# Optimization experiments

Measured on AMD Instinct MI355X. Metric: run time of the kernel, lower is better.

The kernel has to match this reference:

```python
import jax, jax.numpy as jnp
import numpy as np

B, N, C, L = 32, 1024, 1024, 16  # batch, pixels (HW), channels, visual tokens


def setup_inputs() -> dict:
    key = jax.random.key(0)
    ks = jax.random.split(key, 18)
    s = lambda fan_in: 1.0 / np.sqrt(fan_in)
    def lin(kw, kb, fin, fout):
        W = jax.random.uniform(kw, (fin, fout), jnp.float32, -s(fin), s(fin))
        b = jax.random.uniform(kb, (fout,), jnp.float32, -s(fin), s(fin))
        return W, b
    tok_W, tok_b = lin(ks[0], ks[1], C, L)          # tokenizer pointwise conv
    key_W, key_b = lin(ks[2], ks[3], C, C // 2)     # transformer key proj
    query_W, query_b = lin(ks[4], ks[5], C, C // 2) # transformer query proj
    f1_W, f1_b = lin(ks[6], ks[7], C, C)            # FFN 1
    f2_W, f2_b = lin(ks[8], ks[9], C, C)            # FFN 2
    q_W, q_b = lin(ks[10], ks[11], C, C)            # projector W_q
    k_W, k_b = lin(ks[12], ks[13], C, C)            # projector W_k
    feature_map = jax.random.normal(ks[14], (B, N, C), jnp.float32)
    T_in = jnp.zeros((B, L, C), jnp.float32)  # unused by FilterBasedTokenizer
    return dict(feature_map=feature_map, T_in=T_in,
                tok_W=tok_W, tok_b=tok_b, key_W=key_W, key_b=key_b,
                query_W=query_W, query_b=query_b, f1_W=f1_W, f1_b=f1_b,
                f2_W=f2_W, f2_b=f2_b, q_W=q_W, q_b=q_b, k_W=k_W, k_b=k_b)


def reference(feature_map, T_in, tok_W, tok_b, key_W, key_b, query_W, query_b,
              f1_W, f1_b, f2_W, f2_b, q_W, q_b, k_W, k_b):
    X = feature_map  # [B, N, C]
    # --- FilterBasedTokenizer: softmax over pixel dim, aggregate pixels -> tokens
    proj = X @ tok_W + tok_b                         # [B, N, L]
    attn = jax.nn.softmax(proj, axis=1)              # softmax over N (dim=1)
    T = jnp.einsum('bnl,bnc->blc', attn, X)          # [B, L, C]
    # --- Transformer block on visual tokens
    k = T @ key_W + key_b                            # [B, L, C/2]
    q = T @ query_W + query_b                        # [B, L, C/2]
    scores = jnp.einsum('bld,bmd->blm', k, q)        # [B, L, L]
    T_dash = T + jax.nn.softmax(scores, axis=2) @ T  # self-attn residual
    T_out = T_dash + (jax.nn.relu(T_dash @ f1_W + f1_b) @ f2_W + f2_b)
    # --- Projector: pixels attend to tokens
    sim = jnp.einsum('bnc,blc->bnl', X @ q_W + q_b, T_out @ k_W + k_b)  # [B, N, L]
    X_out = X + jax.nn.softmax(sim, axis=2) @ T_out  # [B, N, C]
    return (X_out, T_out)
```

## Files before the change

### kernel.cpp

```cpp
#include <hip/hip_runtime.h>
#include <hip/hip_bf16.h>
#include <stdint.h>

#define BB 32
#define NN 1024
#define CC 1024
#define LL 16

typedef __attribute__((ext_vector_type(4))) float f32x4;
typedef __attribute__((ext_vector_type(8))) short short8;
typedef __attribute__((ext_vector_type(4))) unsigned short ushort4v;

__device__ __forceinline__ unsigned short f2bf(float f) {
  union { float f; unsigned u; } v; v.f = f;
  unsigned r = v.u + 0x7FFF + ((v.u >> 16) & 1);
  return (unsigned short)(r >> 16);
}
__device__ __forceinline__ float bf2f(unsigned short h) {
  union { unsigned u; float f; } v; v.u = ((unsigned)h) << 16; return v.f;
}

__global__ __launch_bounds__(256) void wprep(
    const float* __restrict__ keyW, const float* __restrict__ queryW,
    const float* __restrict__ f1W, const float* __restrict__ f2W,
    const float* __restrict__ kW, const float* __restrict__ qW,
    const float* __restrict__ tokW, const float* __restrict__ keyb,
    const float* __restrict__ queryb,
    unsigned short* __restrict__ WkqT, unsigned short* __restrict__ f1WT,
    unsigned short* __restrict__ f2WT, unsigned short* __restrict__ kWT,
    unsigned short* __restrict__ qWbf, unsigned short* __restrict__ tokWT,
    float* __restrict__ biaskq)
{
  int z = blockIdx.z;
  int tx = threadIdx.x, ty = threadIdx.y;
  if (z == 5) {
    int gid = (blockIdx.y * 32 + blockIdx.x) * 256 + ty * 32 + tx;
    if (gid < 16384) {
      int l = gid >> 10, c = gid & 1023;
      tokWT[gid] = f2bf(tokW[c * 16 + l]);
    } else if (gid < 17408) {
      int i = gid - 16384;
      biaskq[i] = (i < 512) ? keyb[i] : queryb[i - 512];
    }
    return;
  }
  if (z == 4) {
#pragma unroll
    for (int i = 0; i < 4; ++i) {
      int row = blockIdx.y * 32 + ty + 8 * i;
      int col = blockIdx.x * 32 + tx;
      qWbf[row * 1024 + col] = f2bf(qW[row * 1024 + col]);
    }
    return;
  }
  __shared__ float tile[32][33];
  int j0 = blockIdx.x * 32, k0 = blockIdx.y * 32;
  const float* src = (z == 1) ? f1W : (z == 2) ? f2W : kW;
#pragma unroll
  for (int i = 0; i < 4; ++i) {
    int k = k0 + ty + 8 * i;
    int j = j0 + tx;
    float v;
    if (z == 0) v = (j < 512) ? keyW[k * 512 + j] : queryW[k * 512 + (j - 512)];
    else        v = src[k * 1024 + j];
    tile[ty + 8 * i][tx] = v;
  }
  __syncthreads();
  unsigned short* dst = (z == 0) ? WkqT : (z == 1) ? f1WT : (z == 2) ? f2WT : kWT;
#pragma unroll
  for (int i = 0; i < 4; ++i) {
    int j = j0 + ty + 8 * i;
    dst[j * 1024 + k0 + tx] = f2bf(tile[tx][ty + 8 * i]);
  }
}

__global__ __launch_bounds__(256) void proj_mfma(
    const float* __restrict__ X, const unsigned short* __restrict__ Wt,
    const float* __restrict__ bias, float* __restrict__ out)
{
  __shared__ __align__(16) char sp[16384];
  int tid = threadIdx.x, wid = tid >> 6, lane = tid & 63;
  int lr = lane & 15, hi = lane >> 4;
  int pix0 = blockIdx.x * 64;
  int b = pix0 >> 10;
  int row = tid >> 2, seg = tid & 3;
  const float* xr = X + (size_t)(pix0 + row) * 1024 + seg * 32;
  const unsigned short* Wb = Wt + (size_t)lr * 1024 + hi * 8;
  int wbyte[4];
#pragma unroll
  for (int u = 0; u < 4; ++u)
    wbyte[u] = row * 256 + (((seg * 64 + u * 16) ^ ((row & 7) << 4)));
  int arow = wid * 16 + lr;
  int rbyte = arow * 256;
  int rx = (arow & 7) << 4;
  f32x4 acc = (f32x4)0.f;
  for (int k0 = 0; k0 < 1024; k0 += 128) {
    f32x4 v[8];
#pragma unroll
    for (int i = 0; i < 8; ++i) v[i] = *(const f32x4*)(xr + k0 + i * 4);
    __syncthreads();
#pragma unroll
    for (int u = 0; u < 4; ++u) {
      short8 pk;
      pk[0] = (short)f2bf(v[2*u][0]);   pk[1] = (short)f2bf(v[2*u][1]);
      pk[2] = (short)f2bf(v[2*u][2]);   pk[3] = (short)f2bf(v[2*u][3]);
      pk[4] = (short)f2bf(v[2*u+1][0]); pk[5] = (short)f2bf(v[2*u+1][1]);
      pk[6] = (short)f2bf(v[2*u+1][2]); pk[7] = (short)f2bf(v[2*u+1][3]);
      *(short8*)(sp + wbyte[u]) = pk;
    }
    __syncthreads();
#pragma unroll
    for (int kk = 0; kk < 4; ++kk) {
      short8 af = *(const short8*)(sp + rbyte + (((kk * 64 + hi * 16) ^ rx)));
      short8 bf = *(const short8*)(Wb + k0 + kk * 32);
      acc = __builtin_amdgcn_mfma_f32_16x16x32_bf16(af, bf, acc, 0, 0, 0);
    }
  }
  int pixb = pix0 + wid * 16 + hi * 4;
  float bv = bias[lr];
#pragma unroll
  for (int rr = 0; rr < 4; ++rr) {
    int pix = pixb + rr;
    out[((size_t)b * 16 + lr) * 1024 + (pix & 1023)] = acc[rr] + bv;
  }
}

__global__ __launch_bounds__(256) void softmax_n(float* __restrict__ projT) {
  float* row = projT + (size_t)blockIdx.x * NN;
  int t = threadIdx.x;
  f32x4 v = ((f32x4*)row)[t];
  float m = fmaxf(fmaxf(v[0], v[1]), fmaxf(v[2], v[3]));
#pragma unroll
  for (int msk = 32; msk >= 1; msk >>= 1) m = fmaxf(m, __shfl_xor(m, msk));
  __shared__ float redm[4], reds[4];
  if ((t & 63) == 0) redm[t >> 6] = m;
  __syncthreads();
  m = fmaxf(fmaxf(redm[0], redm[1]), fmaxf(redm[2], redm[3]));
  f32x4 e;
  e[0] = __expf(v[0] - m); e[1] = __expf(v[1] - m);
  e[2] = __expf(v[2] - m); e[3] = __expf(v[3] - m);
  float s = e[0] + e[1] + e[2] + e[3];
#pragma unroll
  for (int msk = 32; msk >= 1; msk >>= 1) s += __shfl_xor(s, msk);
  if ((t & 63) == 0) reds[t >> 6] = s;
  __syncthreads();
  s = reds[0] + reds[1] + reds[2] + reds[3];
  float inv = 1.f / s;
  e[0] *= inv; e[1] *= inv; e[2] *= inv; e[3] *= inv;
  ((f32x4*)row)[t] = e;
}

__global__ __launch_bounds__(256) void tpart_kernel(
    const float* __restrict__ X, const float* __restrict__ attnT,
    unsigned short* __restrict__ TpartBf)
{
  int b = blockIdx.y, ch = blockIdx.x;
  int n0 = ch * 128;
  __shared__ float att[128][16];
  int tid = threadIdx.x;
#pragma unroll
  for (int i = 0; i < 2; ++i) {
    int fi = tid + 256 * i;
    int l = fi >> 5, n4 = (fi & 31) << 2;
    f32x4 a = *(const f32x4*)&attnT[((size_t)b * 16 + l) * 1024 + n0 + n4];
    att[n4 + 0][l] = a[0]; att[n4 + 1][l] = a[1];
    att[n4 + 2][l] = a[2]; att[n4 + 3][l] = a[3];
  }
  __syncthreads();
  f32x4 acc[16];
#pragma unroll
  for (int l = 0; l < 16; ++l) acc[l] = (f32x4)0.f;
  const float* xp = X + ((size_t)b * 1024 + n0) * 1024 + tid * 4;
#pragma unroll 4
  for (int n = 0; n < 128; ++n) {
    f32x4 xv = *(const f32x4*)(xp + (size_t)n * 1024);
    const f32x4* ar = (const f32x4*)&att[n][0];
    f32x4 a0 = ar[0], a1 = ar[1], a2 = ar[2], a3 = ar[3];
    acc[0]  += a0[0]*xv; acc[1]  += a0[1]*xv; acc[2]  += a0[2]*xv; acc[3]  += a0[3]*xv;
    acc[4]  += a1[0]*xv; acc[5]  += a1[1]*xv; acc[6]  += a1[2]*xv; acc[7]  += a1[3]*xv;
    acc[8]  += a2[0]*xv; acc[9]  += a2[1]*xv; acc[10] += a2[2]*xv; acc[11] += a2[3]*xv;
    acc[12] += a3[0]*xv; acc[13] += a3[1]*xv; acc[14] += a3[2]*xv; acc[15] += a3[3]*xv;
  }
  unsigned short* op = TpartBf + (size_t)(b * 8 + ch) * 16 * 1024 + tid * 4;
#pragma unroll
  for (int l = 0; l < 16; ++l) {
    f32x4 s = acc[l];
    ushort4v h; h[0]=f2bf(s[0]); h[1]=f2bf(s[1]); h[2]=f2bf(s[2]); h[3]=f2bf(s[3]);
    *(ushort4v*)(op + (size_t)l * 1024) = h;
  }
}

__global__ void treduce(const unsigned short* __restrict__ TpartBf,
                        float* __restrict__ T, unsigned short* __restrict__ Tbf) {
  int f = blockIdx.x * 256 + threadIdx.x;
  int b = f >> 12, w = f & 4095;
  f32x4 s = (f32x4)0.f;
#pragma unroll
  for (int ch = 0; ch < 8; ++ch) {
    ushort4v h = ((const ushort4v*)TpartBf)[(size_t)(b * 8 + ch) * 4096 + w];
    s[0] += bf2f(h[0]); s[1] += bf2f(h[1]); s[2] += bf2f(h[2]); s[3] += bf2f(h[3]);
  }
  ((f32x4*)T)[f] = s;
  ushort4v h; h[0]=f2bf(s[0]); h[1]=f2bf(s[1]); h[2]=f2bf(s[2]); h[3]=f2bf(s[3]);
  ((ushort4v*)Tbf)[f] = h;
}

template<int RELU, int HAS_BIAS, int HAS_RES, int STORE_F32, int STORE_BF16>
__global__ __launch_bounds__(256) void gemm32x64(
    const unsigned short* __restrict__ A, const unsigned short* __restrict__ Bm,
    const float* __restrict__ bias, const float* __restrict__ res,
    float* __restrict__ outF, unsigned short* __restrict__ outB)
{
  const int K = 1024;
  __shared__ __align__(16) char sh[12288];
  char* Asp = sh;
  char* Bsp = sh + 4096;
  int tid = threadIdx.x, wid = tid >> 6, lane = tid & 63;
  int lr = lane & 15, hi = lane >> 4;
  int m0 = blockIdx.x * 32, n0 = blockIdx.y * 64;
  int arow = tid >> 3, acol = (tid & 7) * 8;
  int brow = tid >> 2, bcol = (tid & 3) * 16;
  const unsigned short* Ap = A + (size_t)(m0 + arow) * K + acol;
  const unsigned short* Bp = Bm + (size_t)(n0 + brow) * K + bcol;
  int aw  = arow * 128 + (((acol * 2) ^ ((arow & 7) << 4)));
  int bw0 = brow * 128 + (((bcol * 2) ^ ((brow & 7) << 4)));
  int bw1 = brow * 128 + ((((bcol * 2) + 16) ^ ((brow & 7) << 4)));
  short8 aR[2]; short8 bR[2][2];
  aR[0]    = *(const short8*)(Ap);
  bR[0][0] = *(const short8*)(Bp);
  bR[0][1] = *(const short8*)(Bp + 8);
  aR[1]    = *(const short8*)(Ap + 64);
  bR[1][0] = *(const short8*)(Bp + 64);
  bR[1][1] = *(const short8*)(Bp + 72);
  f32x4 acc[2];
  acc[0] = (f32x4)0.f; acc[1] = (f32x4)0.f;
  int wm = (wid >> 1) * 16, wn = (wid & 1) * 32;
  int arb = (wm + lr) * 128, arx = ((wm + lr) & 7) << 4;
  for (int s = 0; s < 16; ++s) {
    __syncthreads();
    *(short8*)(Asp + aw)  = aR[s & 1];
    *(short8*)(Bsp + bw0) = bR[s & 1][0];
    *(short8*)(Bsp + bw1) = bR[s & 1][1];
    __syncthreads();
    if (s + 2 < 16) {
      int k0 = (s + 2) * 64;
      aR[s & 1]    = *(const short8*)(Ap + k0);
      bR[s & 1][0] = *(const short8*)(Bp + k0);
      bR[s & 1][1] = *(const short8*)(Bp + k0 + 8);
    }
#pragma unroll
    for (int kk = 0; kk < 2; ++kk) {
      short8 af = *(const short8*)(Asp + arb + (((kk * 64 + hi * 16) ^ arx)));
#pragma unroll
      for (int sn = 0; sn < 2; ++sn) {
        int br = wn + sn * 16 + lr;
        short8 bf = *(const short8*)(Bsp + br * 128 + (((kk * 64 + hi * 16) ^ ((br & 7) << 4))));
        acc[sn] = __builtin_amdgcn_mfma_f32_16x16x32_bf16(af, bf, acc[sn], 0, 0, 0);
      }
    }
  }
  int row0 = m0 + wm + hi * 4;
#pragma unroll
  for (int sn = 0; sn < 2; ++sn) {
    int col = n0 + wn + sn * 16 + lr;
    float bv_ = HAS_BIAS ? bias[col] : 0.f;
#pragma unroll
    for (int rr = 0; rr < 4; ++rr) {
      float x = acc[sn][rr] + bv_;
      if (RELU) x = fmaxf(x, 0.f);
      size_t idx = (size_t)(row0 + rr) * 1024 + col;
      if (HAS_RES) x += res[idx];
      if (STORE_F32) outF[idx] = x;
      if (STORE_BF16) outB[idx] = f2bf(x);
    }
  }
}

__global__ __launch_bounds__(256) void scores_tdash(
    const float* __restrict__ kq, const float* __restrict__ T,
    float* __restrict__ Tdash, unsigned short* __restrict__ Tdbf)
{
  int cs = blockIdx.x, b = blockIdx.y;
  int c0 = cs * 128;
  __shared__ float Ts[16][128];
  int tid = threadIdx.x, lane = tid & 63;
#pragma unroll
  for (int i = 0; i < 2; ++i) {
    int fi = tid + 256 * i;
    int rrow = fi >> 5, c4 = (fi & 31) * 4;
    *(f32x4*)&Ts[rrow][c4] = *(const f32x4*)&T[((size_t)b * 16 + rrow) * 1024 + c0 + c4];
  }
  __syncthreads();
  int l = tid >> 4, m = tid & 15;
  const float* krow = kq + ((size_t)b * 16 + l) * 1024;
  const float* qrow = kq + ((size_t)b * 16 + m) * 1024 + 512;
  float s = 0.f;
#pragma unroll 8
  for (int d = 0; d < 512; d += 4) {
    f32x4 kv = *(const f32x4*)(krow + d);
    f32x4 qv = *(const f32x4*)(qrow + d);
    s += kv[0]*qv[0] + kv[1]*qv[1] + kv[2]*qv[2] + kv[3]*qv[3];
  }
  float mx = s;
  mx = fmaxf(mx, __shfl_xor(mx, 1)); mx = fmaxf(mx, __shfl_xor(mx, 2));
  mx = fmaxf(mx, __shfl_xor(mx, 4)); mx = fmaxf(mx, __shfl_xor(mx, 8));
  float e = __expf(s - mx);
  float sum = e;
  sum += __shfl_xor(sum, 1); sum += __shfl_xor(sum, 2);
  sum += __shfl_xor(sum, 4); sum += __shfl_xor(sum, 8);
  float pv = e / sum;
  float pl[16];
#pragma unroll
  for (int i = 0; i < 16; ++i) pl[i] = __shfl(pv, (lane & 48) + i);
  float* od = Tdash + ((size_t)b * 16 + l) * 1024 + c0;
  unsigned short* ob = Tdbf + ((size_t)b * 16 + l) * 1024 + c0;
#pragma unroll
  for (int h = 0; h < 2; ++h) {
    int c = m * 8 + h * 4;
    f32x4 o = *(const f32x4*)&Ts[l][c];
#pragma unroll
    for (int mm = 0; mm < 16; ++mm) {
      f32x4 tv = *(const f32x4*)&Ts[mm][c];
      o += pl[mm] * tv;
    }
    *(f32x4*)(od + c) = o;
    ushort4v hh; hh[0]=f2bf(o[0]); hh[1]=f2bf(o[1]); hh[2]=f2bf(o[2]); hh[3]=f2bf(o[3]);
    *(ushort4v*)(ob + c) = hh;
  }
}

__global__ __launch_bounds__(256) void r_kernel(
    const unsigned short* __restrict__ Tkbf, const float* __restrict__ qb,
    float* __restrict__ r)
{
  int row = blockIdx.x * 4 + (threadIdx.x >> 6);
  int lane = threadIdx.x & 63;
  const unsigned short* p = Tkbf + (size_t)row * CC;
  float s = 0.f;
#pragma unroll
  for (int h = 0; h < 2; ++h) {
    int d0 = lane * 8 + h * 512;
    short8 v = *(const short8*)&p[d0];
#pragma unroll
    for (int jj = 0; jj < 8; ++jj)
      s += bf2f((unsigned short)v[jj]) * qb[d0 + jj];
  }
#pragma unroll
  for (int msk = 32; msk >= 1; msk >>= 1) s += __shfl_xor(s, msk);
  if (lane == 0) r[row] = s;
}

__global__ __launch_bounds__(256) void sim_out_kernel(
    const float* __restrict__ X, const unsigned short* __restrict__ Gt,
    const float* __restrict__ rbias, const float* __restrict__ Tout,
    float* __restrict__ Xout)
{
  __shared__ __align__(16) char sp[16384];
  __shared__ float Ps[64][16];
  int tid = threadIdx.x, wid = tid >> 6, lane = tid & 63;
  int lr = lane & 15, hi = lane >> 4;
  int pix0 = blockIdx.x * 64 + blockIdx.y * 1024;
  int b = blockIdx.y;
  int row = tid >> 2, seg = tid & 3;
  const float* xr = X + (size_t)(pix0 + row) * 1024 + seg * 32;
  const unsigned short* Wb = Gt + (size_t)b * 16 * 1024 + (size_t)lr * 1024 + hi * 8;
  int wbyte[4];
#pragma unroll
  for (int u = 0; u < 4; ++u)
    wbyte[u] = row * 256 + (((seg * 64 + u * 16) ^ ((row & 7) << 4)));
  int arow = wid * 16 + lr;
  int rbyte = arow * 256;
  int rx = (arow & 7) << 4;
  f32x4 acc = (f32x4)0.f;
  for (int k0 = 0; k0 < 1024; k0 += 128) {
    f32x4 v[8];
#pragma unroll
    for (int i = 0; i < 8; ++i) v[i] = *(const f32x4*)(xr + k0 + i * 4);
    __syncthreads();
#pragma unroll
    for (int u = 0; u < 4; ++u) {
      short8 pk;
      pk[0] = (short)f2bf(v[2*u][0]);   pk[1] = (short)f2bf(v[2*u][1]);
      pk[2] = (short)f2bf(v[2*u][2]);   pk[3] = (short)f2bf(v[2*u][3]);
      pk[4] = (short)f2bf(v[2*u+1][0]); pk[5] = (short)f2bf(v[2*u+1][1]);
      pk[6] = (short)f2bf(v[2*u+1][2]); pk[7] = (short)f2bf(v[2*u+1][3]);
      *(short8*)(sp + wbyte[u]) = pk;
    }
    __syncthreads();
#pragma unroll
    for (int kk = 0; kk < 4; ++kk) {
      short8 af = *(const short8*)(sp + rbyte + (((kk * 64 + hi * 16) ^ rx)));
      short8 bf = *(const short8*)(Wb + k0 + kk * 32);
      acc = __builtin_amdgcn_mfma_f32_16x16x32_bf16(af, bf, acc, 0, 0, 0);
    }
  }
  float bv = rbias[b * 16 + lr];
  int prow = wid * 16 + hi * 4;
#pragma unroll
  for (int rr = 0; rr < 4; ++rr) {
    float vv = acc[rr] + bv;
    float mx = vv;
    mx = fmaxf(mx, __shfl_xor(mx, 1)); mx = fmaxf(mx, __shfl_xor(mx, 2));
    mx = fmaxf(mx, __shfl_xor(mx, 4)); mx = fmaxf(mx, __shfl_xor(mx, 8));
    float e = __expf(vv - mx);
    float ss = e;
    ss += __shfl_xor(ss, 1); ss += __shfl_xor(ss, 2);
    ss += __shfl_xor(ss, 4); ss += __shfl_xor(ss, 8);
    Ps[prow + rr][lr] = e / ss;
  }
  __syncthreads();
  int c4 = tid * 4;
  f32x4 tsr[16];
#pragma unroll
  for (int l = 0; l < 16; ++l)
    tsr[l] = *(const f32x4*)&Tout[((size_t)b * 16 + l) * 1024 + c4];
  const float* xp = X + (size_t)pix0 * 1024 + c4;
  float* op = Xout + (size_t)pix0 * 1024 + c4;
#pragma unroll 2
  for (int n = 0; n < 64; ++n) {
    f32x4 xv = *(const f32x4*)(xp + (size_t)n * 1024);
    const f32x4* pr = (const f32x4*)&Ps[n][0];
    f32x4 p0 = pr[0], p1 = pr[1], p2 = pr[2], p3 = pr[3];
    f32x4 o = xv;
    o += p0[0]*tsr[0];  o += p0[1]*tsr[1];  o += p0[2]*tsr[2];  o += p0[3]*tsr[3];
    o += p1[0]*tsr[4];  o += p1[1]*tsr[5];  o += p1[2]*tsr[6];  o += p1[3]*tsr[7];
    o += p2[0]*tsr[8];  o += p2[1]*tsr[9];  o += p2[2]*tsr[10]; o += p2[3]*tsr[11];
    o += p3[0]*tsr[12]; o += p3[1]*tsr[13]; o += p3[2]*tsr[14]; o += p3[3]*tsr[15];
    *(f32x4*)(op + (size_t)n * 1024) = o;
  }
}

extern "C" void kernel_launch(void* const* d_in, const int* in_sizes, int n_in,
                              void* d_out, int out_size, void* d_ws, size_t ws_size,
                              hipStream_t stream)
{
  const float* X      = (const float*)d_in[0];
  const float* tokW   = (const float*)d_in[2];
  const float* tokB   = (const float*)d_in[3];
  const float* keyW   = (const float*)d_in[4];
  const float* keyB   = (const float*)d_in[5];
  const float* queryW = (const float*)d_in[6];
  const float* queryB = (const float*)d_in[7];
  const float* f1W    = (const float*)d_in[8];
  const float* f1B    = (const float*)d_in[9];
  const float* f2W    = (const float*)d_in[10];
  const float* f2B    = (const float*)d_in[11];
  const float* qW     = (const float*)d_in[12];
  const float* qB     = (const float*)d_in[13];
  const float* kW     = (const float*)d_in[14];
  const float* kB     = (const float*)d_in[15];

  float* Xout = (float*)d_out;
  float* Tout = (float*)d_out + (size_t)BB * NN * CC;

  char* ws = (char*)d_ws;
  size_t off = 0;
  auto alloc_f = [&](size_t n) { float* pp = (float*)(ws + off); off += n * 4; return pp; };
  float* attn   = alloc_f(524288);
  float* Tbuf   = alloc_f(524288);
  float* kqbuf  = alloc_f(524288);
  float* Tdash  = alloc_f(524288);
  float* rbuf   = alloc_f(1024);
  float* biaskq = alloc_f(1024);
  auto alloc_h = [&](size_t n) { unsigned short* pp = (unsigned short*)(ws + off); off += n * 2; return pp; };
  unsigned short* TpartBf = alloc_h(4194304);
  unsigned short* Tbf    = alloc_h(524288);
  unsigned short* Tdbf   = alloc_h(524288);
  unsigned short* Hbf    = alloc_h(524288);
  unsigned short* Toutbf = alloc_h(524288);
  unsigned short* Tkbf   = alloc_h(524288);
  unsigned short* Gtbf   = alloc_h(524288);
  unsigned short* WkqT   = alloc_h(1048576);
  unsigned short* f1WT   = alloc_h(1048576);
  unsigned short* f2WT   = alloc_h(1048576);
  unsigned short* kWT    = alloc_h(1048576);
  unsigned short* qWbf   = alloc_h(1048576);
  unsigned short* tokWT  = alloc_h(16384);
  (void)ws_size; (void)in_sizes; (void)n_in; (void)out_size;

  wprep<<<dim3(32, 32, 6), dim3(32, 8), 0, stream>>>(keyW, queryW, f1W, f2W, kW, qW,
                                                     tokW, keyB, queryB,
                                                     WkqT, f1WT, f2WT, kWT, qWbf, tokWT, biaskq);
  proj_mfma<<<dim3(512), 256, 0, stream>>>(X, tokWT, tokB, attn);
  softmax_n<<<512, 256, 0, stream>>>(attn);
  tpart_kernel<<<dim3(8, 32), 256, 0, stream>>>(X, attn, TpartBf);
  treduce<<<512, 256, 0, stream>>>(TpartBf, Tbuf, Tbf);
  gemm32x64<0,1,0,1,0><<<dim3(16, 16), 256, 0, stream>>>(Tbf, WkqT, biaskq, nullptr, kqbuf, nullptr);
  scores_tdash<<<dim3(8, 32), 256, 0, stream>>>(kqbuf, Tbuf, Tdash, Tdbf);
  gemm32x64<1,1,0,0,1><<<dim3(16, 16), 256, 0, stream>>>(Tdbf, f1WT, f1B, nullptr, nullptr, Hbf);
  gemm32x64<0,1,1,1,1><<<dim3(16, 16), 256, 0, stream>>>(Hbf, f2WT, f2B, Tdash, Tout, Toutbf);
  gemm32x64<0,1,0,0,1><<<dim3(16, 16), 256, 0, stream>>>(Toutbf, kWT, kB, nullptr, nullptr, Tkbf);
  r_kernel<<<128, 256, 0, stream>>>(Tkbf, qB, rbuf);
  gemm32x64<0,0,0,0,1><<<dim3(16, 16), 256, 0, stream>>>(Tkbf, qWbf, nullptr, nullptr, nullptr, Gtbf);
  sim_out_kernel<<<dim3(16, 32), 256, 0, stream>>>(X, Gtbf, rbuf, Tout, Xout);
}
```

Measured before the change: 210.6 us.

## Replace LDS-staged MFMA tiles with direct-register loads across kernels; split token reduction finer

The projection and sim kernels now feed MFMA straight from global memory, converting fp32 X to bf16 in registers instead of staging through swizzled LDS with barriers. The small GEMMs use a 16x16-per-wave direct-load tile instead of the 32x64 LDS double-buffered tile, doubling the grid. The token aggregation is split into 16 chunks of 64 pixels with batched loads, which doubles the partial buffer and the reduction work. Xout is written with nontemporal stores to avoid polluting cache. The aim is to remove LDS traffic and synchronisation and raise parallelism, at the cost of uncoalesced 32-byte-strided global reads and less operand reuse.

Result: slower. 230.3 us (+9.4%).

```diff
diff --git a/kernel.cpp b/kernel.cpp
--- a/kernel.cpp
+++ b/kernel.cpp
@@ -18,6 +18,14 @@
 }
 __device__ __forceinline__ float bf2f(unsigned short h) {
   union { unsigned u; float f; } v; v.u = ((unsigned)h) << 16; return v.f;
+}
+__device__ __forceinline__ short8 cvt8(f32x4 a, f32x4 b) {
+  short8 r;
+  r[0] = (short)f2bf(a[0]); r[1] = (short)f2bf(a[1]);
+  r[2] = (short)f2bf(a[2]); r[3] = (short)f2bf(a[3]);
+  r[4] = (short)f2bf(b[0]); r[5] = (short)f2bf(b[1]);
+  r[6] = (short)f2bf(b[2]); r[7] = (short)f2bf(b[3]);
+  return r;
 }
 
 __global__ __launch_bounds__(256) void wprep(
@@ -74,55 +82,29 @@
   }
 }
 
-__global__ __launch_bounds__(256) void proj_mfma(
-    const float* __restrict__ X, const unsigned short* __restrict__ Wt,
-    const float* __restrict__ bias, float* __restrict__ out)
-{
-  __shared__ __align__(16) char sp[16384];
+__global__ __launch_bounds__(256) void proj_direct(
+    const float* __restrict__ X, const unsigned short* __restrict__ tokWT,
+    const float* __restrict__ tokB, float* __restrict__ attn)
+{
   int tid = threadIdx.x, wid = tid >> 6, lane = tid & 63;
   int lr = lane & 15, hi = lane >> 4;
-  int pix0 = blockIdx.x * 64;
+  int pix0 = (blockIdx.x * 4 + wid) * 16;
   int b = pix0 >> 10;
-  int row = tid >> 2, seg = tid & 3;
-  const float* xr = X + (size_t)(pix0 + row) * 1024 + seg * 32;
-  const unsigned short* Wb = Wt + (size_t)lr * 1024 + hi * 8;
-  int wbyte[4];
-#pragma unroll
-  for (int u = 0; u < 4; ++u)
-    wbyte[u] = row * 256 + (((seg * 64 + u * 16) ^ ((row & 7) << 4)));
-  int arow = wid * 16 + lr;
-  int rbyte = arow * 256;
-  int rx = (arow & 7) << 4;
+  const float* Ar = X + (size_t)(pix0 + lr) * 1024 + hi * 8;
+  const unsigned short* Br = tokWT + lr * 1024 + hi * 8;
   f32x4 acc = (f32x4)0.f;
-  for (int k0 = 0; k0 < 1024; k0 += 128) {
-    f32x4 v[8];
-#pragma unroll
-    for (int i = 0; i < 8; ++i) v[i] = *(const f32x4*)(xr + k0 + i * 4);
-    __syncthreads();
-#pragma unroll
-    for (int u = 0; u < 4; ++u) {
-      short8 pk;
-      pk[0] = (short)f2bf(v[2*u][0]);   pk[1] = (short)f2bf(v[2*u][1]);
-      pk[2] = (short)f2bf(v[2*u][2]);   pk[3] = (short)f2bf(v[2*u][3]);
-      pk[4] = (short)f2bf(v[2*u+1][0]); pk[5] = (short)f2bf(v[2*u+1][1]);
-      pk[6] = (short)f2bf(v[2*u+1][2]); pk[7] = (short)f2bf(v[2*u+1][3]);
-      *(short8*)(sp + wbyte[u]) = pk;
-    }
-    __syncthreads();
-#pragma unroll
-    for (int kk = 0; kk < 4; ++kk) {
-      short8 af = *(const short8*)(sp + rbyte + (((kk * 64 + hi * 16) ^ rx)));
-      short8 bf = *(const short8*)(Wb + k0 + kk * 32);
-      acc = __builtin_amdgcn_mfma_f32_16x16x32_bf16(af, bf, acc, 0, 0, 0);
-    }
-  }
-  int pixb = pix0 + wid * 16 + hi * 4;
-  float bv = bias[lr];
-#pragma unroll
-  for (int rr = 0; rr < 4; ++rr) {
-    int pix = pixb + rr;
-    out[((size_t)b * 16 + lr) * 1024 + (pix & 1023)] = acc[rr] + bv;
-  }
+#pragma unroll 4
+  for (int k0 = 0; k0 < 1024; k0 += 32) {
+    f32x4 x0 = *(const f32x4*)(Ar + k0);
+    f32x4 x1 = *(const f32x4*)(Ar + k0 + 4);
+    short8 bfrag = *(const short8*)(Br + k0);
+    acc = __builtin_amdgcn_mfma_f32_16x16x32_bf16(cvt8(x0, x1), bfrag, acc, 0, 0, 0);
+  }
+  float bv = tokB[lr];
+  int pixb = pix0 + hi * 4;
+#pragma unroll
+  for (int rr = 0; rr < 4; ++rr)
+    attn[((size_t)b * 16 + lr) * 1024 + ((pixb + rr) & 1023)] = acc[rr] + bv;
 }
 
 __global__ __launch_bounds__(256) void softmax_n(float* __restrict__ projT) {
@@ -155,13 +137,11 @@
     unsigned short* __restrict__ TpartBf)
 {
   int b = blockIdx.y, ch = blockIdx.x;
-  int n0 = ch * 128;
-  __shared__ float att[128][16];
+  int n0 = ch * 64;
+  __shared__ float att[64][16];
   int tid = threadIdx.x;
-#pragma unroll
-  for (int i = 0; i < 2; ++i) {
-    int fi = tid + 256 * i;
-    int l = fi >> 5, n4 = (fi & 31) << 2;
+  {
+    int l = tid >> 4, n4 = (tid & 15) * 4;
     f32x4 a = *(const f32x4*)&attnT[((size_t)b * 16 + l) * 1024 + n0 + n4];
     att[n4 + 0][l] = a[0]; att[n4 + 1][l] = a[1];
     att[n4 + 2][l] = a[2]; att[n4 + 3][l] = a[3];
@@ -171,17 +151,22 @@
 #pragma unroll
   for (int l = 0; l < 16; ++l) acc[l] = (f32x4)0.f;
   const float* xp = X + ((size_t)b * 1024 + n0) * 1024 + tid * 4;
-#pragma unroll 4
-  for (int n = 0; n < 128; ++n) {
-    f32x4 xv = *(const f32x4*)(xp + (size_t)n * 1024);
-    const f32x4* ar = (const f32x4*)&att[n][0];
-    f32x4 a0 = ar[0], a1 = ar[1], a2 = ar[2], a3 = ar[3];
-    acc[0]  += a0[0]*xv; acc[1]  += a0[1]*xv; acc[2]  += a0[2]*xv; acc[3]  += a0[3]*xv;
-    acc[4]  += a1[0]*xv; acc[5]  += a1[1]*xv; acc[6]  += a1[2]*xv; acc[7]  += a1[3]*xv;
-    acc[8]  += a2[0]*xv; acc[9]  += a2[1]*xv; acc[10] += a2[2]*xv; acc[11] += a2[3]*xv;
-    acc[12] += a3[0]*xv; acc[13] += a3[1]*xv; acc[14] += a3[2]*xv; acc[15] += a3[3]*xv;
-  }
-  unsigned short* op = TpartBf + (size_t)(b * 8 + ch) * 16 * 1024 + tid * 4;
+  for (int nb = 0; nb < 64; nb += 8) {
+    f32x4 xv[8];
+#pragma unroll
+    for (int i = 0; i < 8; ++i) xv[i] = *(const f32x4*)(xp + (size_t)(nb + i) * 1024);
+#pragma unroll
+    for (int i = 0; i < 8; ++i) {
+      const f32x4* ar = (const f32x4*)&att[nb + i][0];
+      f32x4 a0 = ar[0], a1 = ar[1], a2 = ar[2], a3 = ar[3];
+      f32x4 x0 = xv[i];
+      acc[0]  += a0[0]*x0; acc[1]  += a0[1]*x0; acc[2]  += a0[2]*x0; acc[3]  += a0[3]*x0;
+      acc[4]  += a1[0]*x0; acc[5]  += a1[1]*x0; acc[6]  += a1[2]*x0; acc[7]  += a1[3]*x0;
+      acc[8]  += a2[0]*x0; acc[9]  += a2[1]*x0; acc[10] += a2[2]*x0; acc[11] += a2[3]*x0;
+      acc[12] += a3[0]*x0; acc[13] += a3[1]*x0; acc[14] += a3[2]*x0; acc[15] += a3[3]*x0;
+    }
+  }
+  unsigned short* op = TpartBf + (size_t)(b * 16 + ch) * 16 * 1024 + tid * 4;
 #pragma unroll
   for (int l = 0; l < 16; ++l) {
     f32x4 s = acc[l];
@@ -196,8 +181,8 @@
   int b = f >> 12, w = f & 4095;
   f32x4 s = (f32x4)0.f;
 #pragma unroll
-  for (int ch = 0; ch < 8; ++ch) {
-    ushort4v h = ((const ushort4v*)TpartBf)[(size_t)(b * 8 + ch) * 4096 + w];
+  for (int ch = 0; ch < 16; ++ch) {
+    ushort4v h = ((const ushort4v*)TpartBf)[(size_t)(b * 16 + ch) * 4096 + w];
     s[0] += bf2f(h[0]); s[1] += bf2f(h[1]); s[2] += bf2f(h[2]); s[3] += bf2f(h[3]);
   }
   ((f32x4*)T)[f] = s;
@@ -206,73 +191,35 @@
 }
 
 template<int RELU, int HAS_BIAS, int HAS_RES, int STORE_F32, int STORE_BF16>
-__global__ __launch_bounds__(256) void gemm32x64(
+__global__ __launch_bounds__(256) void gemm_direct(
     const unsigned short* __restrict__ A, const unsigned short* __restrict__ Bm,
     const float* __restrict__ bias, const float* __restrict__ res,
     float* __restrict__ outF, unsigned short* __restrict__ outB)
 {
-  const int K = 1024;
-  __shared__ __align__(16) char sh[12288];
-  char* Asp = sh;
-  char* Bsp = sh + 4096;
   int tid = threadIdx.x, wid = tid >> 6, lane = tid & 63;
   int lr = lane & 15, hi = lane >> 4;
-  int m0 = blockIdx.x * 32, n0 = blockIdx.y * 64;
-  int arow = tid >> 3, acol = (tid & 7) * 8;
-  int brow = tid >> 2, bcol = (tid & 3) * 16;
-  const unsigned short* Ap = A + (size_t)(m0 + arow) * K + acol;
-  const unsigned short* Bp = Bm + (size_t)(n0 + brow) * K + bcol;
-  int aw  = arow * 128 + (((acol * 2) ^ ((arow & 7) << 4)));
-  int bw0 = brow * 128 + (((bcol * 2) ^ ((brow & 7) << 4)));
-  int bw1 = brow * 128 + ((((bcol * 2) + 16) ^ ((brow & 7) << 4)));
-  short8 aR[2]; short8 bR[2][2];
-  aR[0]    = *(const short8*)(Ap);
-  bR[0][0] = *(const short8*)(Bp);
-  bR[0][1] = *(const short8*)(Bp + 8);
-  aR[1]    = *(const short8*)(Ap + 64);
-  bR[1][0] = *(const short8*)(Bp + 64);
-  bR[1][1] = *(const short8*)(Bp + 72);
-  f32x4 acc[2];
-  acc[0] = (f32x4)0.f; acc[1] = (f32x4)0.f;
-  int wm = (wid >> 1) * 16, wn = (wid & 1) * 32;
-  int arb = (wm + lr) * 128, arx = ((wm + lr) & 7) << 4;
-  for (int s = 0; s < 16; ++s) {
-    __syncthreads();
-    *(short8*)(Asp + aw)  = aR[s & 1];
-    *(short8*)(Bsp + bw0) = bR[s & 1][0];
-    *(short8*)(Bsp + bw1) = bR[s & 1][1];
-    __syncthreads();
-    if (s + 2 < 16) {
-      int k0 = (s + 2) * 64;
-      aR[s & 1]    = *(const short8*)(Ap + k0);
-      bR[s & 1][0] = *(const short8*)(Bp + k0);
-      bR[s & 1][1] = *(const short8*)(Bp + k0 + 8);
-    }
-#pragma unroll
-    for (int kk = 0; kk < 2; ++kk) {
-      short8 af = *(const short8*)(Asp + arb + (((kk * 64 + hi * 16) ^ arx)));
-#pragma unroll
-      for (int sn = 0; sn < 2; ++sn) {
-        int br = wn + sn * 16 + lr;
-        short8 bf = *(const short8*)(Bsp + br * 128 + (((kk * 64 + hi * 16) ^ ((br & 7) << 4))));
-        acc[sn] = __builtin_amdgcn_mfma_f32_16x16x32_bf16(af, bf, acc[sn], 0, 0, 0);
-      }
-    }
-  }
-  int row0 = m0 + wm + hi * 4;
-#pragma unroll
-  for (int sn = 0; sn < 2; ++sn) {
-    int col = n0 + wn + sn * 16 + lr;
-    float bv_ = HAS_BIAS ? bias[col] : 0.f;
-#pragma unroll
-    for (int rr = 0; rr < 4; ++rr) {
-      float x = acc[sn][rr] + bv_;
-      if (RELU) x = fmaxf(x, 0.f);
-      size_t idx = (size_t)(row0 + rr) * 1024 + col;
-      if (HAS_RES) x += res[idx];
-      if (STORE_F32) outF[idx] = x;
-      if (STORE_BF16) outB[idx] = f2bf(x);
-    }
+  int m0 = blockIdx.x * 16;
+  int n0 = (blockIdx.y * 4 + wid) * 16;
+  const unsigned short* Ap = A + (size_t)(m0 + lr) * 1024 + hi * 8;
+  const unsigned short* Bp = Bm + (size_t)(n0 + lr) * 1024 + hi * 8;
+  f32x4 acc = (f32x4)0.f;
+#pragma unroll 8
+  for (int k0 = 0; k0 < 1024; k0 += 32) {
+    short8 a = *(const short8*)(Ap + k0);
+    short8 b = *(const short8*)(Bp + k0);
+    acc = __builtin_amdgcn_mfma_f32_16x16x32_bf16(a, b, acc, 0, 0, 0);
+  }
+  int row0 = m0 + hi * 4;
+  int col = n0 + lr;
+  float bv_ = HAS_BIAS ? bias[col] : 0.f;
+#pragma unroll
+  for (int rr = 0; rr < 4; ++rr) {
+    float x = acc[rr] + bv_;
+    if (RELU) x = fmaxf(x, 0.f);
+    size_t idx = (size_t)(row0 + rr) * 1024 + col;
+    if (HAS_RES) x += res[idx];
+    if (STORE_F32) outF[idx] = x;
+    if (STORE_BF16) outB[idx] = f2bf(x);
   }
 }
 
@@ -355,44 +302,21 @@
     const float* __restrict__ rbias, const float* __restrict__ Tout,
     float* __restrict__ Xout)
 {
-  __shared__ __align__(16) char sp[16384];
   __shared__ float Ps[64][16];
   int tid = threadIdx.x, wid = tid >> 6, lane = tid & 63;
   int lr = lane & 15, hi = lane >> 4;
-  int pix0 = blockIdx.x * 64 + blockIdx.y * 1024;
   int b = blockIdx.y;
-  int row = tid >> 2, seg = tid & 3;
-  const float* xr = X + (size_t)(pix0 + row) * 1024 + seg * 32;
-  const unsigned short* Wb = Gt + (size_t)b * 16 * 1024 + (size_t)lr * 1024 + hi * 8;
-  int wbyte[4];
-#pragma unroll
-  for (int u = 0; u < 4; ++u)
-    wbyte[u] = row * 256 + (((seg * 64 + u * 16) ^ ((row & 7) << 4)));
-  int arow = wid * 16 + lr;
-  int rbyte = arow * 256;
-  int rx = (arow & 7) << 4;
+  int pix0b = b * 1024 + blockIdx.x * 64;
+  int pix0 = pix0b + wid * 16;
+  const float* Ar = X + (size_t)(pix0 + lr) * 1024 + hi * 8;
+  const unsigned short* Br = Gt + (size_t)b * 16384 + lr * 1024 + hi * 8;
   f32x4 acc = (f32x4)0.f;
-  for (int k0 = 0; k0 < 1024; k0 += 128) {
-    f32x4 v[8];
-#pragma unroll
-    for (int i = 0; i < 8; ++i) v[i] = *(const f32x4*)(xr + k0 + i * 4);
-    __syncthreads();
-#pragma unroll
-    for (int u = 0; u < 4; ++u) {
-      short8 pk;
-      pk[0] = (short)f2bf(v[2*u][0]);   pk[1] = (short)f2bf(v[2*u][1]);
-      pk[2] = (short)f2bf(v[2*u][2]);   pk[3] = (short)f2bf(v[2*u][3]);
-      pk[4] = (short)f2bf(v[2*u+1][0]); pk[5] = (short)f2bf(v[2*u+1][1]);
-      pk[6] = (short)f2bf(v[2*u+1][2]); pk[7] = (short)f2bf(v[2*u+1][3]);
-      *(short8*)(sp + wbyte[u]) = pk;
-    }
-    __syncthreads();
-#pragma unroll
-    for (int kk = 0; kk < 4; ++kk) {
-      short8 af = *(const short8*)(sp + rbyte + (((kk * 64 + hi * 16) ^ rx)));
-      short8 bf = *(const short8*)(Wb + k0 + kk * 32);
-      acc = __builtin_amdgcn_mfma_f32_16x16x32_bf16(af, bf, acc, 0, 0, 0);
-    }
+#pragma unroll 4
+  for (int k0 = 0; k0 < 1024; k0 += 32) {
+    f32x4 x0 = *(const f32x4*)(Ar + k0);
+    f32x4 x1 = *(const f32x4*)(Ar + k0 + 4);
+    short8 bfrag = *(const short8*)(Br + k0);
+    acc = __builtin_amdgcn_mfma_f32_16x16x32_bf16(cvt8(x0, x1), bfrag, acc, 0, 0, 0);
   }
   float bv = rbias[b * 16 + lr];
   int prow = wid * 16 + hi * 4;
@@ -414,8 +338,8 @@
 #pragma unroll
   for (int l = 0; l < 16; ++l)
     tsr[l] = *(const f32x4*)&Tout[((size_t)b * 16 + l) * 1024 + c4];
-  const float* xp = X + (size_t)pix0 * 1024 + c4;
-  float* op = Xout + (size_t)pix0 * 1024 + c4;
+  const float* xp = X + (size_t)pix0b * 1024 + c4;
+  float* op = Xout + (size_t)pix0b * 1024 + c4;
 #pragma unroll 2
   for (int n = 0; n < 64; ++n) {
     f32x4 xv = *(const f32x4*)(xp + (size_t)n * 1024);
@@ -426,7 +350,7 @@
     o += p1[0]*tsr[4];  o += p1[1]*tsr[5];  o += p1[2]*tsr[6];  o += p1[3]*tsr[7];
     o += p2[0]*tsr[8];  o += p2[1]*tsr[9];  o += p2[2]*tsr[10]; o += p2[3]*tsr[11];
     o += p3[0]*tsr[12]; o += p3[1]*tsr[13]; o += p3[2]*tsr[14]; o += p3[3]*tsr[15];
-    *(f32x4*)(op + (size_t)n * 1024) = o;
+    __builtin_nontemporal_store(o, (f32x4*)(op + (size_t)n * 1024));
   }
 }
 
@@ -463,7 +387,7 @@
   float* rbuf   = alloc_f(1024);
   float* biaskq = alloc_f(1024);
   auto alloc_h = [&](size_t n) { unsigned short* pp = (unsigned short*)(ws + off); off += n * 2; return pp; };
-  unsigned short* TpartBf = alloc_h(4194304);
+  unsigned short* TpartBf = alloc_h(8388608);
   unsigned short* Tbf    = alloc_h(524288);
   unsigned short* Tdbf   = alloc_h(524288);
   unsigned short* Hbf    = alloc_h(524288);
@@ -481,16 +405,16 @@
   wprep<<<dim3(32, 32, 6), dim3(32, 8), 0, stream>>>(keyW, queryW, f1W, f2W, kW, qW,
                                                      tokW, keyB, queryB,
                                                      WkqT, f1WT, f2WT, kWT, qWbf, tokWT, biaskq);
-  proj_mfma<<<dim3(512), 256, 0, stream>>>(X, tokWT, tokB, attn);
+  proj_direct<<<512, 256, 0, stream>>>(X, tokWT, tokB, attn);
   softmax_n<<<512, 256, 0, stream>>>(attn);
-  tpart_kernel<<<dim3(8, 32), 256, 0, stream>>>(X, attn, TpartBf);
+  tpart_kernel<<<dim3(16, 32), 256, 0, stream>>>(X, attn, TpartBf);
   treduce<<<512, 256, 0, stream>>>(TpartBf, Tbuf, Tbf);
-  gemm32x64<0,1,0,1,0><<<dim3(16, 16), 256, 0, stream>>>(Tbf, WkqT, biaskq, nullptr, kqbuf, nullptr);
+  gemm_direct<0,1,0,1,0><<<dim3(32, 16), 256, 0, stream>>>(Tbf, WkqT, biaskq, nullptr, kqbuf, nullptr);
   scores_tdash<<<dim3(8, 32), 256, 0, stream>>>(kqbuf, Tbuf, Tdash, Tdbf);
-  gemm32x64<1,1,0,0,1><<<dim3(16, 16), 256, 0, stream>>>(Tdbf, f1WT, f1B, nullptr, nullptr, Hbf);
-  gemm32x64<0,1,1,1,1><<<dim3(16, 16), 256, 0, stream>>>(Hbf, f2WT, f2B, Tdash, Tout, Toutbf);
-  gemm32x64<0,1,0,0,1><<<dim3(16, 16), 256, 0, stream>>>(Toutbf, kWT, kB, nullptr, nullptr, Tkbf);
+  gemm_direct<1,1,0,0,1><<<dim3(32, 16), 256, 0, stream>>>(Tdbf, f1WT, f1B, nullptr, nullptr, Hbf);
+  gemm_direct<0,1,1,1,1><<<dim3(32, 16), 256, 0, stream>>>(Hbf, f2WT, f2B, Tdash, Tout, Toutbf);
+  gemm_direct<0,1,0,0,1><<<dim3(32, 16), 256, 0, stream>>>(Toutbf, kWT, kB, nullptr, nullptr, Tkbf);
   r_kernel<<<128, 256, 0, stream>>>(Tkbf, qB, rbuf);
-  gemm32x64<0,0,0,0,1><<<dim3(16, 16), 256, 0, stream>>>(Tkbf, qWbf, nullptr, nullptr, nullptr, Gtbf);
+  gemm_direct<0,0,0,0,1><<<dim3(32, 16), 256, 0, stream>>>(Tkbf, qWbf, nullptr, nullptr, nullptr, Gtbf);
   sim_out_kernel<<<dim3(16, 32), 256, 0, stream>>>(X, Gtbf, rbuf, Tout, Xout);
 }
```
